# Performance work log

Hardware: AMD Instinct MI355X
Metric: run time of the kernel (lower is better)

## Reference

```python
import jax, jax.numpy as jnp
import numpy as np

BLOCK_LEN = 64  # chunk length l


def setup_inputs() -> dict:
    key = jax.random.key(0)
    k1, k2, k3 = jax.random.split(key, 3)
    b, s, h, p, n = 8, 4096, 16, 64, 64
    X = jax.random.normal(k1, (b, s, h, p), jnp.float32)
    # A must be negative for numerically stable decays (exp(cumsum diffs) <= 1),
    # matching real Mamba2 where A_log parameterizes a negative decay rate.
    A = -0.1 * jnp.abs(jax.random.normal(k2, (b, s, h), jnp.float32))
    B = jax.random.normal(k3, (b, s, h, n), jnp.float32)
    return {"X": X, "A": A, "B": B}


def reference(X, A, B):
    L = BLOCK_LEN
    b, s, h, p = X.shape
    n = B.shape[-1]
    c = s // L  # number of chunks

    # b (c l) ... -> b c l ...
    Xb = X.reshape(b, c, L, h, p)
    Bb = B.reshape(b, c, L, h, n)
    Ab = jnp.transpose(A.reshape(b, c, L, h), (0, 3, 1, 2))  # (b, h, c, l)

    A_cumsum = jnp.cumsum(Ab, axis=-1)  # (b, h, c, l)

    # Fused decay-einsum: states[b,c,h,p,n] =
    #   sum_l B[b,c,l,h,n] * exp(A_cumsum[b,h,c,-1] - A_cumsum[b,h,c,l]) * X[b,c,l,h,p]
    decay_states = jnp.exp(A_cumsum[..., -1:] - A_cumsum)  # (b, h, c, l)
    states = jnp.einsum('bclhn,bhcl,bclhp->bchpn', Bb, decay_states, Xb)

    # Prepend zero initial states along chunk dim -> (b, c+1, h, p, n)
    states = jnp.concatenate([jnp.zeros_like(states[:, :1]), states], axis=1)

    # Inter-chunk recurrence via exp(segsum(padded chunk totals)).
    padded_A = jnp.pad(A_cumsum[..., -1], ((0, 0), (0, 0), (1, 0)))  # (b, h, c+1)
    cs = jnp.cumsum(padded_A, axis=-1)
    Z = c + 1
    diff = cs[..., :, None] - cs[..., None, :]  # (b, h, Z, Z), row - col
    mask = jnp.tril(jnp.ones((Z, Z), dtype=bool))  # row >= col
    decay_chunk = jnp.where(mask, jnp.exp(diff), 0.0)  # (b, h, Z, Z)

    new_states = jnp.einsum('bhzc,bchpn->bzhpn', decay_chunk, states)
    return new_states[:, -1]  # (b, h, p, n)
```

## Files before the change

### kernel.cpp

```cpp
#include <hip/hip_runtime.h>


constexpr int Bn = 8;
constexpr int S  = 4096;
constexpr int H  = 16;
constexpr int P  = 64;
constexpr int N  = 64;

constexpr int NCH = 8;
constexpr int TCH = S / NCH;
constexpr int TB  = 32;
constexpr int NIT = TCH / TB;

typedef __attribute__((ext_vector_type(4))) float f32x4;
typedef __attribute__((ext_vector_type(8))) short short8;

__global__ __launch_bounds__(256) void scan_weights(
    const float* __restrict__ A, float* __restrict__ W) {
  const int pair = blockIdx.x;
  const int bb = pair / H, hh = pair % H;
  const int tid = threadIdx.x;
  constexpr int TPT = S / 256;

  float vals[TPT];
  float local = 0.f;
  const int t0 = tid * TPT;
  #pragma unroll
  for (int i = 0; i < TPT; ++i) {
    float a = A[((size_t)bb * S + t0 + i) * H + hh];
    local += a;
    vals[i] = local;
  }

  __shared__ float sums[256];
  sums[tid] = local;
  __syncthreads();
  for (int off = 1; off < 256; off <<= 1) {
    float v = sums[tid];
    float add = (tid >= off) ? sums[tid - off] : 0.f;
    __syncthreads();
    sums[tid] = v + add;
    __syncthreads();
  }
  const float total = sums[255];
  const float excl  = sums[tid] - local;

  float* Wp = W + (size_t)pair * S;
  #pragma unroll
  for (int i = 0; i < TPT; ++i) {
    Wp[t0 + i] = __expf(total - (excl + vals[i]));
  }
}

__device__ __forceinline__ unsigned pack_hilo(float x) {
  unsigned bx = __float_as_uint(x);
  unsigned hi = bx >> 16;
  float rf = x - __uint_as_float(bx & 0xFFFF0000u);
  unsigned lo = __float_as_uint(rf) & 0xFFFF0000u;
  return hi | lo;
}

__device__ __forceinline__ short8 mk_frag(unsigned a0, unsigned a1,
                                          unsigned a2, unsigned a3) {
  union { unsigned u[4]; short8 s; } u;
  u.u[0] = a0; u.u[1] = a1; u.u[2] = a2; u.u[3] = a3;
  return u.s;
}

__global__ __launch_bounds__(256) void outer_accum(
    const float* __restrict__ X, const float* __restrict__ Bm,
    const float* __restrict__ W, float* __restrict__ out) {
  __shared__ unsigned Xl[64 * 33];
  __shared__ unsigned Bl[64 * 33];

  const int bid  = blockIdx.x;
  const int pair = bid / NCH;
  const int ch   = bid % NCH;
  const int tid  = threadIdx.x;
  const int lane = tid & 63;
  const int wid  = __builtin_amdgcn_readfirstlane(tid >> 6);
  const int t_begin = ch * TCH;

  const int bb = pair / H, hh = pair % H;
  constexpr int HP = H * P;
  constexpr int HN = H * N;

  const float* gXc = X  + (size_t)bb * S * HP + (size_t)hh * P + lane;
  const float* gBc = Bm + (size_t)bb * S * HN + (size_t)hh * N + lane;
  const float* Wp  = W + (size_t)pair * S;

  const int m0 = (wid & 1) * 32;
  const int n0 = (wid >> 1) * 32;
  const int l15 = lane & 15;
  const int l4  = lane >> 4;

  f32x4 acc[2][2];
  #pragma unroll
  for (int mt = 0; mt < 2; ++mt)
    #pragma unroll
    for (int nt = 0; nt < 2; ++nt) acc[mt][nt] = (f32x4)0.f;

  for (int it = 0; it < NIT; ++it) {
    const int tb = t_begin + it * TB;
    const int tw = tb + wid * 8;

    float xr[8], br[8], wv[8];
    #pragma unroll
    for (int k = 0; k < 8; ++k) {
      xr[k] = gXc[(size_t)(tw + k) * HP];
      br[k] = gBc[(size_t)(tw + k) * HN];
      wv[k] = Wp[tw + k];
    }

    const int trow = wid * 8;
    #pragma unroll
    for (int k = 0; k < 8; ++k) {
      Xl[lane * 33 + trow + k] = pack_hilo(xr[k] * wv[k]);
      Bl[lane * 33 + trow + k] = pack_hilo(br[k]);
    }
    __syncthreads();

    unsigned ca[2][8], cb[2][8];
    #pragma unroll
    for (int mt = 0; mt < 2; ++mt) {
      const int base = (m0 + mt * 16 + l15) * 33 + l4 * 8;
      #pragma unroll
      for (int j = 0; j < 8; ++j) ca[mt][j] = Xl[base + j];
    }
    #pragma unroll
    for (int nt = 0; nt < 2; ++nt) {
      const int base = (n0 + nt * 16 + l15) * 33 + l4 * 8;
      #pragma unroll
      for (int j = 0; j < 8; ++j) cb[nt][j] = Bl[base + j];
    }

    short8 ahi[2], alo[2], bhi[2], blo[2];
    #pragma unroll
    for (int mt = 0; mt < 2; ++mt) {
      ahi[mt] = mk_frag(__builtin_amdgcn_perm(ca[mt][1], ca[mt][0], 0x05040100),
                        __builtin_amdgcn_perm(ca[mt][3], ca[mt][2], 0x05040100),
                        __builtin_amdgcn_perm(ca[mt][5], ca[mt][4], 0x05040100),
                        __builtin_amdgcn_perm(ca[mt][7], ca[mt][6], 0x05040100));
      alo[mt] = mk_frag(__builtin_amdgcn_perm(ca[mt][1], ca[mt][0], 0x07060302),
                        __builtin_amdgcn_perm(ca[mt][3], ca[mt][2], 0x07060302),
                        __builtin_amdgcn_perm(ca[mt][5], ca[mt][4], 0x07060302),
                        __builtin_amdgcn_perm(ca[mt][7], ca[mt][6], 0x07060302));
    }
    #pragma unroll
    for (int nt = 0; nt < 2; ++nt) {
      bhi[nt] = mk_frag(__builtin_amdgcn_perm(cb[nt][1], cb[nt][0], 0x05040100),
                        __builtin_amdgcn_perm(cb[nt][3], cb[nt][2], 0x05040100),
                        __builtin_amdgcn_perm(cb[nt][5], cb[nt][4], 0x05040100),
                        __builtin_amdgcn_perm(cb[nt][7], cb[nt][6], 0x05040100));
      blo[nt] = mk_frag(__builtin_amdgcn_perm(cb[nt][1], cb[nt][0], 0x07060302),
                        __builtin_amdgcn_perm(cb[nt][3], cb[nt][2], 0x07060302),
                        __builtin_amdgcn_perm(cb[nt][5], cb[nt][4], 0x07060302),
                        __builtin_amdgcn_perm(cb[nt][7], cb[nt][6], 0x07060302));
    }

    #pragma unroll
    for (int mt = 0; mt < 2; ++mt)
      #pragma unroll
      for (int nt = 0; nt < 2; ++nt) {
        f32x4 c = acc[mt][nt];
        c = __builtin_amdgcn_mfma_f32_16x16x32_bf16(alo[mt], bhi[nt], c, 0, 0, 0);
        c = __builtin_amdgcn_mfma_f32_16x16x32_bf16(ahi[mt], blo[nt], c, 0, 0, 0);
        c = __builtin_amdgcn_mfma_f32_16x16x32_bf16(ahi[mt], bhi[nt], c, 0, 0, 0);
        acc[mt][nt] = c;
      }
    __syncthreads();
  }

  float* outp = out + (size_t)pair * P * N;
  #pragma unroll
  for (int mt = 0; mt < 2; ++mt)
    #pragma unroll
    for (int nt = 0; nt < 2; ++nt) {
      const int p = m0 + mt * 16 + l4 * 4;
      const int n = n0 + nt * 16 + l15;
      #pragma unroll
      for (int r = 0; r < 4; ++r)
        atomicAdd(&outp[(size_t)(p + r) * N + n], acc[mt][nt][r]);
    }
}

extern "C" void kernel_launch(void* const* d_in, const int* in_sizes, int n_in,
                              void* d_out, int out_size, void* d_ws, size_t ws_size,
                              hipStream_t stream) {
  const float* X = (const float*)d_in[0];
  const float* A = (const float*)d_in[1];
  const float* B = (const float*)d_in[2];
  float* out = (float*)d_out;
  float* W   = (float*)d_ws;

  hipMemsetAsync(d_out, 0, (size_t)out_size * sizeof(float), stream);

  scan_weights<<<Bn * H, 256, 0, stream>>>(A, W);
  outer_accum<<<Bn * H * NCH, 256, 0, stream>>>(X, B, W, out);
}
```

Before: 296.1 us.

## Double-buffer LDS tiles and prefetch next chunk into registers during MFMA

Splits the shared-memory tiles into two buffers and issues the global loads for the next 32-timestep block before the current block's MFMAs, packing them into the other buffer afterwards. One barrier per iteration is dropped, and global-load latency is meant to overlap with LDS reads and matrix math. The decay weights are also loaded as two float4 vectors instead of scalar loads. This doubles LDS use and raises register pressure, which may reduce occupancy.

```diff
diff --git a/kernel.cpp b/kernel.cpp
--- a/kernel.cpp
+++ b/kernel.cpp
@@ -67,11 +67,40 @@
   return u.s;
 }
 
+#define LOADREG(tt0)                                                      \
+  do {                                                                    \
+    const int tw_ = (tt0) + wid * 8;       \
+    w0 = *(const float4*)(Wp + tw_);                                      \
+    w1 = *(const float4*)(Wp + tw_ + 4);                                  \
+    xr[0] = gXc[(size_t)(tw_ + 0) * HP]; br[0] = gBc[(size_t)(tw_ + 0) * HN]; \
+    xr[1] = gXc[(size_t)(tw_ + 1) * HP]; br[1] = gBc[(size_t)(tw_ + 1) * HN]; \
+    xr[2] = gXc[(size_t)(tw_ + 2) * HP]; br[2] = gBc[(size_t)(tw_ + 2) * HN]; \
+    xr[3] = gXc[(size_t)(tw_ + 3) * HP]; br[3] = gBc[(size_t)(tw_ + 3) * HN]; \
+    xr[4] = gXc[(size_t)(tw_ + 4) * HP]; br[4] = gBc[(size_t)(tw_ + 4) * HN]; \
+    xr[5] = gXc[(size_t)(tw_ + 5) * HP]; br[5] = gBc[(size_t)(tw_ + 5) * HN]; \
+    xr[6] = gXc[(size_t)(tw_ + 6) * HP]; br[6] = gBc[(size_t)(tw_ + 6) * HN]; \
+    xr[7] = gXc[(size_t)(tw_ + 7) * HP]; br[7] = gBc[(size_t)(tw_ + 7) * HN]; \
+  } while (0)
+
+#define PACKSTORE(buf)                                                    \
+  do {                                                                    \
+    unsigned* Xd_ = &Xl[buf][lane * 33 + wid * 8];                        \
+    unsigned* Bd_ = &Bl[buf][lane * 33 + wid * 8];                        \
+    Xd_[0] = pack_hilo(xr[0] * w0.x);  Bd_[0] = pack_hilo(br[0]);         \
+    Xd_[1] = pack_hilo(xr[1] * w0.y);  Bd_[1] = pack_hilo(br[1]);         \
+    Xd_[2] = pack_hilo(xr[2] * w0.z);  Bd_[2] = pack_hilo(br[2]);         \
+    Xd_[3] = pack_hilo(xr[3] * w0.w);  Bd_[3] = pack_hilo(br[3]);         \
+    Xd_[4] = pack_hilo(xr[4] * w1.x);  Bd_[4] = pack_hilo(br[4]);         \
+    Xd_[5] = pack_hilo(xr[5] * w1.y);  Bd_[5] = pack_hilo(br[5]);         \
+    Xd_[6] = pack_hilo(xr[6] * w1.z);  Bd_[6] = pack_hilo(br[6]);         \
+    Xd_[7] = pack_hilo(xr[7] * w1.w);  Bd_[7] = pack_hilo(br[7]);         \
+  } while (0)
+
 __global__ __launch_bounds__(256) void outer_accum(
     const float* __restrict__ X, const float* __restrict__ Bm,
     const float* __restrict__ W, float* __restrict__ out) {
-  __shared__ unsigned Xl[64 * 33];
-  __shared__ unsigned Bl[64 * 33];
+  __shared__ unsigned Xl[2][64 * 33];
+  __shared__ unsigned Bl[2][64 * 33];
 
   const int bid  = blockIdx.x;
   const int pair = bid / NCH;
@@ -100,38 +129,31 @@
     #pragma unroll
     for (int nt = 0; nt < 2; ++nt) acc[mt][nt] = (f32x4)0.f;
 
+  float xr[8], br[8];
+  float4 w0, w1;
+
+  LOADREG(t_begin);
+  PACKSTORE(0);
+  __syncthreads();
+
   for (int it = 0; it < NIT; ++it) {
-    const int tb = t_begin + it * TB;
-    const int tw = tb + wid * 8;
-
-    float xr[8], br[8], wv[8];
-    #pragma unroll
-    for (int k = 0; k < 8; ++k) {
-      xr[k] = gXc[(size_t)(tw + k) * HP];
-      br[k] = gBc[(size_t)(tw + k) * HN];
-      wv[k] = Wp[tw + k];
-    }
-
-    const int trow = wid * 8;
-    #pragma unroll
-    for (int k = 0; k < 8; ++k) {
-      Xl[lane * 33 + trow + k] = pack_hilo(xr[k] * wv[k]);
-      Bl[lane * 33 + trow + k] = pack_hilo(br[k]);
-    }
-    __syncthreads();
-
+    const int cur = it & 1;
+    if (it + 1 < NIT) LOADREG(t_begin + (it + 1) * TB);
+
+    const unsigned* Xc = &Xl[cur][0];
+    const unsigned* Bc = &Bl[cur][0];
     unsigned ca[2][8], cb[2][8];
     #pragma unroll
     for (int mt = 0; mt < 2; ++mt) {
       const int base = (m0 + mt * 16 + l15) * 33 + l4 * 8;
       #pragma unroll
-      for (int j = 0; j < 8; ++j) ca[mt][j] = Xl[base + j];
+      for (int j = 0; j < 8; ++j) ca[mt][j] = Xc[base + j];
     }
     #pragma unroll
     for (int nt = 0; nt < 2; ++nt) {
       const int base = (n0 + nt * 16 + l15) * 33 + l4 * 8;
       #pragma unroll
-      for (int j = 0; j < 8; ++j) cb[nt][j] = Bl[base + j];
+      for (int j = 0; j < 8; ++j) cb[nt][j] = Bc[base + j];
     }
 
     short8 ahi[2], alo[2], bhi[2], blo[2];
@@ -168,6 +190,8 @@
         c = __builtin_amdgcn_mfma_f32_16x16x32_bf16(ahi[mt], bhi[nt], c, 0, 0, 0);
         acc[mt][nt] = c;
       }
+
+    if (it + 1 < NIT) PACKSTORE(cur ^ 1);
     __syncthreads();
   }
 
```

Result: no change. 295.4 us (-0.3%).
